# Optimization experiments

Measured on AMD Instinct MI355X. Metric: run time of the kernel, lower is better.

## Reference

```python
import jax, jax.numpy as jnp
import numpy as np

HEADS = 8
DIM_HEAD = 64
CHUNK = 128
EPS = 1e-6
KERNEL_EPS = 1e-4


def softmax_kernel(x, proj, is_query):
    # x: [b,h,n,d], proj: [f,d]  (FAVOR+ positive softmax features)
    d = x.shape[-1]
    data_normalizer = d ** -0.25
    ratio = proj.shape[0] ** -0.5
    data_dash = jnp.einsum('bhnd,fd->bhnf', x * data_normalizer, proj)
    diag = 0.5 * (data_normalizer ** 2) * jnp.sum(x * x, axis=-1, keepdims=True)  # [b,h,n,1]
    if is_query:
        m = jnp.max(data_dash, axis=-1, keepdims=True)
    else:
        m = jnp.max(data_dash, axis=(-1, -2), keepdims=True)
    return ratio * (jnp.exp(data_dash - diag - jax.lax.stop_gradient(m)) + KERNEL_EPS)


def infer_hidden_states(q, k, v, chunk_size=CHUNK):
    # q,k: [b,h,n,f], v: [b,h,n,e]; chunked causal linear attention with carried cumsums
    b, h, n, f = q.shape
    e = v.shape[-1]
    nc = n // chunk_size

    def to_chunks(t):
        return jnp.moveaxis(t.reshape(b, h, nc, chunk_size, t.shape[-1]), 2, 0)

    qs, ks, vs = to_chunks(q), to_chunks(k), to_chunks(v)

    def step(carry, inp):
        Z, S = carry  # [b,h,1,f], [b,h,1,f,e]
        qc, kc, vc = inp
        k_cum = Z + jnp.cumsum(kc, axis=2)                       # [b,h,c,f]
        D_inv = 1.0 / jnp.einsum('bhnf,bhnf->bhn', qc, k_cum + EPS)
        ctx = jnp.einsum('bhnf,bhne->bhnfe', kc, vc)             # [b,h,c,f,e]
        ctx_cum = S + jnp.cumsum(ctx, axis=2)
        out = jnp.einsum('bhnfe,bhnf,bhn->bhne', ctx_cum, qc, D_inv)
        return (k_cum[:, :, -1:], ctx_cum[:, :, -1:]), out

    init = (jnp.zeros((b, h, 1, f), q.dtype), jnp.zeros((b, h, 1, f, e), q.dtype))
    (Z, S), outs = jax.lax.scan(step, init, (qs, ks, vs))
    out = jnp.moveaxis(outs, 0, 2).reshape(b, h, n, e)
    return out, Z[:, :, 0], S[:, :, 0]


def reference(x, proj, Wq, Wk, Wv, Wo, bo):
    b, n, dim = x.shape
    h, dh = HEADS, DIM_HEAD

    def split_heads(t):
        return jnp.transpose(t.reshape(b, n, h, dh), (0, 2, 1, 3))

    q = split_heads(x @ Wq)
    k = split_heads(x @ Wk)
    v = split_heads(x @ Wv)

    qf = softmax_kernel(q, proj, is_query=True)
    kf = softmax_kernel(k, proj, is_query=False)

    out, Z, S = infer_hidden_states(qf, kf, v)
    out = jnp.transpose(out, (0, 2, 1, 3)).reshape(b, n, h * dh)
    out = out @ Wo + bo
    return out, Z, S


def setup_inputs() -> dict:
    key = jax.random.key(0)
    ks = jax.random.split(key, 6)
    b, n, dim = 2, 2048, 512
    f = 256
    return {
        'x': jax.random.normal(ks[0], (b, n, dim), jnp.float32),
        'proj': jax.random.normal(ks[1], (f, DIM_HEAD), jnp.float32),
        'Wq': jax.random.normal(ks[2], (dim, dim), jnp.float32) * (dim ** -0.5),
        'Wk': jax.random.normal(ks[3], (dim, dim), jnp.float32) * (dim ** -0.5),
        'Wv': jax.random.normal(ks[4], (dim, dim), jnp.float32) * (dim ** -0.5),
        'Wo': jax.random.normal(ks[5], (dim, dim), jnp.float32) * (dim ** -0.5),
        'bo': jnp.zeros((dim,), jnp.float32),
    }
```

## Files before the change

### kernel.cpp

```cpp
#include <hip/hip_runtime.h>
#include <hip/hip_bf16.h>
#include <math.h>

#define NB    2
#define NSEQ  2048
#define DIMM  512
#define NH    8
#define DHd   64
#define FF    256
#define CHK   128
#define NCHK  16
#define NBH   16

typedef unsigned short ushort_t;
typedef __attribute__((ext_vector_type(8))) __bf16 bf16x8;
typedef __attribute__((ext_vector_type(4))) float floatx4;

__device__ __forceinline__ unsigned short f2bf(float x) {
    union { __hip_bfloat16 h; unsigned short u; } v;
    v.h = __float2bfloat16(x);
    return v.u;
}
__device__ __forceinline__ float bf2f(unsigned short u) {
    union { unsigned short u2[2]; float f; } v;
    v.u2[0] = 0; v.u2[1] = u;
    return v.f;
}
__device__ __forceinline__ unsigned enc_f(float x) {
    unsigned u = __float_as_uint(x);
    return (u & 0x80000000u) ? ~u : (u | 0x80000000u);
}
__device__ __forceinline__ float dec_f(unsigned e) {
    unsigned u = (e & 0x80000000u) ? (e & 0x7fffffffu) : ~e;
    return __uint_as_float(u);
}

__device__ __forceinline__ void gload16(const void* g, void* l) {
    __builtin_amdgcn_global_load_lds(
        (const __attribute__((address_space(1))) void*)g,
        (__attribute__((address_space(3))) void*)l, 16, 0, 0);
}

__device__ __forceinline__ bf16x8 frag8(const ushort_t* lds, int row, int kb) {
    return *((const bf16x8*)lds + row * 8 + (kb ^ (row & 7)));
}
__device__ __forceinline__ bf16x8 fragS(const ushort_t* lds, int row, int kb) {
    return *((const bf16x8*)lds + row * 16 + (kb ^ (row & 15)));
}

__global__ __launch_bounds__(256)
void prep(const float* __restrict__ x, const float* __restrict__ proj,
          const float* __restrict__ W0, const float* __restrict__ W1,
          const float* __restrict__ W2, const float* __restrict__ W3,
          ushort_t* __restrict__ xb, ushort_t* __restrict__ projb,
          ushort_t* __restrict__ T0, ushort_t* __restrict__ T1,
          ushort_t* __restrict__ T2, ushort_t* __restrict__ T3,
          unsigned* __restrict__ mk_u)
{
    __shared__ float t[32][33];
    const int b = blockIdx.x, tid = threadIdx.x;
    if (b < 2048) {
        const int gid = b * 256 + tid;
        const float4 v = *(const float4*)(x + (size_t)gid * 4);
        union { ushort4 v4; unsigned short s[4]; } pk;
        pk.s[0] = f2bf(v.x); pk.s[1] = f2bf(v.y); pk.s[2] = f2bf(v.z); pk.s[3] = f2bf(v.w);
        ((ushort4*)xb)[gid] = pk.v4;
    } else if (b < 2064) {
        const int gid = (b - 2048) * 256 + tid;
        const float dn = 0.35355339059327379f;
        const float4 v = *(const float4*)(proj + (size_t)gid * 4);
        union { ushort4 v4; unsigned short s[4]; } pk;
        pk.s[0] = f2bf(v.x * dn); pk.s[1] = f2bf(v.y * dn);
        pk.s[2] = f2bf(v.z * dn); pk.s[3] = f2bf(v.w * dn);
        ((ushort4*)projb)[gid] = pk.v4;
    } else if (b < 3088) {
        const int idx = b - 2064;
        const int z = idx >> 8, rem = idx & 255;
        const int bx = rem & 15, by = rem >> 4;
        const float* W = (z == 0) ? W0 : (z == 1) ? W1 : (z == 2) ? W2 : W3;
        ushort_t* T = (z == 0) ? T0 : (z == 1) ? T1 : (z == 2) ? T2 : T3;
        const int x0 = bx * 32, y0 = by * 32;
        const int tx = tid & 31, ty = tid >> 5;
#pragma unroll
        for (int i = 0; i < 4; i++)
            t[ty + i * 8][tx] = W[(size_t)(y0 + ty + i * 8) * DIMM + x0 + tx];
        __syncthreads();
#pragma unroll
        for (int i = 0; i < 4; i++)
            T[(size_t)(x0 + ty + i * 8) * DIMM + y0 + tx] = f2bf(t[tx][ty + i * 8]);
    } else {
        if (tid < NBH) mk_u[tid] = 0u;
    }
}

__device__ __forceinline__ void mfma_mainloop(
    const ushort_t* __restrict__ AG, const ushort_t* __restrict__ BG,
    ushort_t* As, ushort_t* Bs, int ldA, int ldB, int K,
    floatx4 acc[4][4], int tid)
{
    const int lane = tid & 63, wid = tid >> 6;
    const int q = lane >> 4, c = lane & 15;
    const int wm = (wid >> 1) * 64, wn = (wid & 1) * 64;

    for (int k0 = 0; k0 < K; k0 += 64) {
#pragma unroll
        for (int t = 0; t < 4; t++) {
            const int g = t * 256 + tid, r = g >> 3, kb = (g & 7) ^ (r & 7);
            gload16(AG + (size_t)r * ldA + k0 + kb * 8, As + (size_t)g * 8);
        }
#pragma unroll
        for (int t = 0; t < 4; t++) {
            const int g = t * 256 + tid, r = g >> 3, kb = (g & 7) ^ (r & 7);
            gload16(BG + (size_t)r * ldB + k0 + kb * 8, Bs + (size_t)g * 8);
        }
        __syncthreads();
#pragma unroll
        for (int ks = 0; ks < 2; ks++) {
            bf16x8 af[4], bfr[4];
#pragma unroll
            for (int i = 0; i < 4; i++) {
                af[i]  = frag8(As, wm + i * 16 + c, ks * 4 + q);
                bfr[i] = frag8(Bs, wn + i * 16 + c, ks * 4 + q);
            }
#pragma unroll
            for (int i = 0; i < 4; i++)
#pragma unroll
                for (int j = 0; j < 4; j++)
                    acc[i][j] = __builtin_amdgcn_mfma_f32_16x16x32_bf16(
                        af[i], bfr[j], acc[i][j], 0, 0, 0);
        }
        __syncthreads();
    }
}

__global__ __launch_bounds__(256)
void gemm_qkv(const ushort_t* __restrict__ xb,
              const ushort_t* __restrict__ Wtq, const ushort_t* __restrict__ Wtk,
              const ushort_t* __restrict__ Wtv,
              ushort_t* __restrict__ qb, ushort_t* __restrict__ kb,
              ushort_t* __restrict__ vTb)
{
    __shared__ alignas(16) ushort_t SM[16640];
    ushort_t* As = SM;
    ushort_t* Bs = SM + 8192;
    const int tid = threadIdx.x;
    const int n0 = blockIdx.x * 128, m0 = blockIdx.y * 128, z = blockIdx.z;
    const ushort_t* Bt = (z == 0) ? Wtq : ((z == 1) ? Wtk : Wtv);

    floatx4 zero = {0.f, 0.f, 0.f, 0.f};
    floatx4 acc[4][4];
#pragma unroll
    for (int i = 0; i < 4; i++)
#pragma unroll
        for (int j = 0; j < 4; j++) acc[i][j] = zero;

    mfma_mainloop(xb + (size_t)m0 * DIMM, Bt + (size_t)n0 * DIMM, As, Bs,
                  DIMM, DIMM, DIMM, acc, tid);

    const int lane = tid & 63, wid = tid >> 6;
    const int q = lane >> 4, c = lane & 15;
    const int wm = (wid >> 1) * 64, wn = (wid & 1) * 64;
    if (z < 2) {
        ushort_t* ob = (z == 0) ? qb : kb;
#pragma unroll
        for (int i = 0; i < 4; i++)
#pragma unroll
            for (int j = 0; j < 4; j++) {
                const int col = n0 + wn + j * 16 + c;
#pragma unroll
                for (int r = 0; r < 4; r++) {
                    const int row = m0 + wm + i * 16 + q * 4 + r;
                    ob[(size_t)row * DIMM + col] = f2bf(acc[i][j][r]);
                }
            }
    } else {
#pragma unroll
        for (int i = 0; i < 4; i++)
#pragma unroll
            for (int j = 0; j < 4; j++) {
                const int col = wn + j * 16 + c;
#pragma unroll
                for (int r = 0; r < 4; r++) {
                    const int row = wm + i * 16 + q * 4 + r;
                    SM[row * 130 + col] = f2bf(acc[i][j][r]);
                }
            }
        __syncthreads();
        const int bb = m0 >> 11, nbase = m0 & 2047;
#pragma unroll
        for (int p = 0; p < 16; p++) {
            const int idx = p * 256 + tid;
            const int cl2 = idx >> 5, n4 = idx & 31;
            const int C = n0 + cl2;
            const int h = C >> 6, e = C & 63;
            union { ushort4 v4; unsigned short s[4]; } pk;
#pragma unroll
            for (int k = 0; k < 4; k++) pk.s[k] = SM[(n4 * 4 + k) * 130 + cl2];
            *(ushort4*)(vTb + (((size_t)(bb * NH + h) * 64 + e)) * NSEQ + nbase + n4 * 4) = pk.v4;
        }
    }
}

__global__ __launch_bounds__(256)
void gemm_out(const ushort_t* __restrict__ attnb, const ushort_t* __restrict__ Wto,
              float* __restrict__ out, const float* __restrict__ bias)
{
    __shared__ alignas(16) ushort_t As[8192];
    __shared__ alignas(16) ushort_t Bs[8192];
    const int tid = threadIdx.x;
    const int n0 = blockIdx.x * 128, m0 = blockIdx.y * 128;

    floatx4 zero = {0.f, 0.f, 0.f, 0.f};
    floatx4 acc[4][4];
#pragma unroll
    for (int i = 0; i < 4; i++)
#pragma unroll
        for (int j = 0; j < 4; j++) acc[i][j] = zero;

    mfma_mainloop(attnb + (size_t)m0 * DIMM, Wto + (size_t)n0 * DIMM, As, Bs,
                  DIMM, DIMM, DIMM, acc, tid);

    const int lane = tid & 63, wid = tid >> 6;
    const int q = lane >> 4, c = lane & 15;
    const int wm = (wid >> 1) * 64, wn = (wid & 1) * 64;
#pragma unroll
    for (int i = 0; i < 4; i++)
#pragma unroll
        for (int j = 0; j < 4; j++) {
            const int col = n0 + wn + j * 16 + c;
            const float bv = bias[col];
#pragma unroll
            for (int r = 0; r < 4; r++) {
                const int row = m0 + wm + i * 16 + q * 4 + r;
                out[(size_t)row * DIMM + col] = acc[i][j][r] + bv;
            }
        }
}

__global__ __launch_bounds__(256)
void feat_qk(const ushort_t* __restrict__ qb_, const ushort_t* __restrict__ kb_,
             const ushort_t* __restrict__ projb,
             ushort_t* __restrict__ qfb, float* __restrict__ ddk,
             unsigned* __restrict__ mk_u)
{
    __shared__ alignas(16) ushort_t As[8192];
    __shared__ alignas(16) ushort_t Bs[16384];
    __shared__ float dtmp[256];
    __shared__ float diag_l[128];
    __shared__ float mx2[2][128];
    __shared__ float red[256];
    const int tid = threadIdx.x, lane = tid & 63, wid = tid >> 6;
    const int q = lane >> 4, cl = lane & 15;
    const int m0 = blockIdx.x * 128, h = blockIdx.y, src = blockIdx.z;
    const int bb = m0 >> 11, nloc = m0 & 2047;
    const ushort_t* Aq = (src ? kb_ : qb_) + (size_t)m0 * DIMM + h * 64;

    if (src == 0) {
        const int row = tid >> 1, half = tid & 1;
        float s = 0.f;
        const ushort_t* p = Aq + (size_t)row * DIMM + half * 32;
#pragma unroll
        for (int d = 0; d < 32; d += 4) {
            ushort4 w = *(const ushort4*)(p + d);
            float a = bf2f(w.x), b2 = bf2f(w.y), c2 = bf2f(w.z), d2 = bf2f(w.w);
            s += a * a + b2 * b2 + c2 * c2 + d2 * d2;
        }
        dtmp[tid] = s;
        __syncthreads();
        if (tid < 128) diag_l[tid] = (dtmp[tid * 2] + dtmp[tid * 2 + 1]) * 0.0625f;
    }

    floatx4 zero = {0.f, 0.f, 0.f, 0.f};
    floatx4 acc[4][8];
#pragma unroll
    for (int i = 0; i < 4; i++)
#pragma unroll
        for (int j = 0; j < 8; j++) acc[i][j] = zero;

    const int wm = (wid >> 1) * 64, wn = (wid & 1) * 128;
#pragma unroll
    for (int t = 0; t < 4; t++) {
        const int g = t * 256 + tid, r = g >> 3, kb = (g & 7) ^ (r & 7);
        gload16(Aq + (size_t)r * DIMM + kb * 8, As + (size_t)g * 8);
    }
#pragma unroll
    for (int t = 0; t < 8; t++) {
        const int g = t * 256 + tid, r = g >> 3, kb = (g & 7) ^ (r & 7);
        gload16(projb + (size_t)r * 64 + kb * 8, Bs + (size_t)g * 8);
    }
    __syncthreads();
#pragma unroll
    for (int ks = 0; ks < 2; ks++) {
        bf16x8 af[4], bfr[8];
#pragma unroll
        for (int i = 0; i < 4; i++) af[i] = frag8(As, wm + i * 16 + cl, ks * 4 + q);
#pragma unroll
        for (int j = 0; j < 8; j++) bfr[j] = frag8(Bs, wn + j * 16 + cl, ks * 4 + q);
#pragma unroll
        for (int i = 0; i < 4; i++)
#pragma unroll
            for (int j = 0; j < 8; j++)
                acc[i][j] = __builtin_amdgcn_mfma_f32_16x16x32_bf16(
                    af[i], bfr[j], acc[i][j], 0, 0, 0);
    }

    if (src == 0) {
#pragma unroll
        for (int i = 0; i < 4; i++)
#pragma unroll
            for (int r = 0; r < 4; r++) {
                const int row = wm + i * 16 + q * 4 + r;
                float mx = -3.0e38f;
#pragma unroll
                for (int j = 0; j < 8; j++) mx = fmaxf(mx, acc[i][j][r]);
                mx = fmaxf(mx, __shfl_xor(mx, 1)); mx = fmaxf(mx, __shfl_xor(mx, 2));
                mx = fmaxf(mx, __shfl_xor(mx, 4)); mx = fmaxf(mx, __shfl_xor(mx, 8));
                if (cl == 0) mx2[wid & 1][row] = mx;
            }
        __syncthreads();
#pragma unroll
        for (int i = 0; i < 4; i++)
#pragma unroll
            for (int r = 0; r < 4; r++) {
                const int row = wm + i * 16 + q * 4 + r;
                const float cc = diag_l[row] + fmaxf(mx2[0][row], mx2[1][row]);
#pragma unroll
                for (int j = 0; j < 8; j++) {
                    const int col = wn + j * 16 + cl;
                    const float v = 0.0625f * (__expf(acc[i][j][r] - cc) + 1.0e-4f);
                    qfb[((size_t)(bb * NH + h) * NSEQ + (nloc + row)) * FF + col] = f2bf(v);
                }
            }
    } else {
        float mloc = -3.0e38f;
#pragma unroll
        for (int i = 0; i < 4; i++)
#pragma unroll
            for (int j = 0; j < 8; j++) {
                const int f = wn + j * 16 + cl;
#pragma unroll
                for (int r = 0; r < 4; r++) {
                    const int row = wm + i * 16 + q * 4 + r;
                    const float v = acc[i][j][r];
                    mloc = fmaxf(mloc, v);
                    ddk[((size_t)(bb * NH + h) * NSEQ + (nloc + row)) * FF + f] = v;
                }
            }
        red[tid] = mloc;
        __syncthreads();
        for (int s = 128; s > 0; s >>= 1) {
            if (tid < s) red[tid] = fmaxf(red[tid], red[tid + s]);
            __syncthreads();
        }
        if (tid == 0) atomicMax(&mk_u[bb * NH + h], enc_f(red[0]));
    }
}

__global__ __launch_bounds__(256)
void exp_tk(const float* __restrict__ ddk, const ushort_t* __restrict__ kb_,
            const unsigned* __restrict__ mk_u,
            ushort_t* __restrict__ kfb, ushort_t* __restrict__ kfTb,
            float* __restrict__ Ksum)
{
    __shared__ ushort_t t[64][136];
    __shared__ float red[4][64];
    __shared__ float dtmp[256];
    __shared__ float diag_l[128];
    const int tid = threadIdx.x;
    const int f0 = blockIdx.x * 64, c = blockIdx.y, bh = blockIdx.z;
    const int bb = bh >> 3, h = bh & 7;
    const int n0 = c * CHK;
    const float m = dec_f(mk_u[bh]);

    {
        const int row = tid >> 1, half = tid & 1;
        float s = 0.f;
        const ushort_t* p = kb_ + (size_t)(bb * NSEQ + n0 + row) * DIMM + h * 64 + half * 32;
#pragma unroll
        for (int d = 0; d < 32; d += 4) {
            ushort4 w = *(const ushort4*)(p + d);
            float a = bf2f(w.x), b2 = bf2f(w.y), c2 = bf2f(w.z), d2 = bf2f(w.w);
            s += a * a + b2 * b2 + c2 * c2 + d2 * d2;
        }
        dtmp[tid] = s;
    }
    __syncthreads();
    if (tid < 128) diag_l[tid] = (dtmp[tid * 2] + dtmp[tid * 2 + 1]) * 0.0625f;
    __syncthreads();

#pragma unroll
    for (int p = 0; p < 8; p++) {
        const int idx = p * 256 + tid;
        const int row = idx >> 4, c4 = idx & 15;
        const float4 d4 = *(const float4*)(ddk + ((size_t)(bh * NSEQ + n0 + row)) * FF + f0 + c4 * 4);
        const float cc = diag_l[row] + m;
        union { ushort4 v4; unsigned short s[4]; } pk;
        pk.s[0] = f2bf(0.0625f * (__expf(d4.x - cc) + 1.0e-4f));
        pk.s[1] = f2bf(0.0625f * (__expf(d4.y - cc) + 1.0e-4f));
        pk.s[2] = f2bf(0.0625f * (__expf(d4.z - cc) + 1.0e-4f));
        pk.s[3] = f2bf(0.0625f * (__expf(d4.w - cc) + 1.0e-4f));
        *(ushort4*)(kfb + ((size_t)(bh * NSEQ + n0 + row)) * FF + f0 + c4 * 4) = pk.v4;
        t[c4 * 4 + 0][row] = pk.s[0]; t[c4 * 4 + 1][row] = pk.s[1];
        t[c4 * 4 + 2][row] = pk.s[2]; t[c4 * 4 + 3][row] = pk.s[3];
    }
    __syncthreads();
    {
        const int f = tid & 63, grp = tid >> 6;
        float s = 0.f;
#pragma unroll
        for (int n = 0; n < 32; n++) s += bf2f(t[f][grp * 32 + n]);
        red[grp][f] = s;
    }
    __syncthreads();
    if (tid < 64)
        Ksum[((size_t)bh * NCHK + c) * FF + f0 + tid] =
            red[0][tid] + red[1][tid] + red[2][tid] + red[3][tid];
#pragma unroll
    for (int p = 0; p < 8; p++) {
        const int idx = p * 256 + tid;
        const int f = idx >> 5, n4 = idx & 31;
        ushort4 o = *(const ushort4*)&t[f][n4 * 4];
        *(ushort4*)(kfTb + ((size_t)(bh * FF + f0 + f)) * NSEQ + n0 + n4 * 4) = o;
    }
}

__global__ __launch_bounds__(256)
void ctx_mfma(const ushort_t* __restrict__ vTb, const ushort_t* __restrict__ kfTb,
              float* __restrict__ CTXT)
{
    __shared__ alignas(16) ushort_t As[4096];
    __shared__ alignas(16) ushort_t Bs[16384];
    const int tid = threadIdx.x, lane = tid & 63, wid = tid >> 6;
    const int q = lane >> 4, cl = lane & 15;
    const int bh = blockIdx.x >> 4, c = blockIdx.x & 15;
    const ushort_t* A = vTb + ((size_t)bh * 64) * NSEQ + c * CHK;
    const ushort_t* B = kfTb + ((size_t)bh * FF) * NSEQ + c * CHK;
    const int fw = wid * 64;

    floatx4 zero = {0.f, 0.f, 0.f, 0.f};
    floatx4 acc[4][4];
#pragma unroll
    for (int i = 0; i < 4; i++)
#pragma unroll
        for (int j = 0; j < 4; j++) acc[i][j] = zero;

    for (int k0 = 0; k0 < CHK; k0 += 64) {
#pragma unroll
        for (int t = 0; t < 2; t++) {
            const int g = t * 256 + tid, r = g >> 3, kb = (g & 7) ^ (r & 7);
            gload16(A + (size_t)r * NSEQ + k0 + kb * 8, As + (size_t)g * 8);
        }
#pragma unroll
        for (int t = 0; t < 8; t++) {
            const int g = t * 256 + tid, r = g >> 3, kb = (g & 7) ^ (r & 7);
            gload16(B + (size_t)r * NSEQ + k0 + kb * 8, Bs + (size_t)g * 8);
        }
        __syncthreads();
#pragma unroll
        for (int ks = 0; ks < 2; ks++) {
            bf16x8 af[4], bfr[4];
#pragma unroll
            for (int i = 0; i < 4; i++) {
                af[i]  = frag8(As, i * 16 + cl, ks * 4 + q);
                bfr[i] = frag8(Bs, fw + i * 16 + cl, ks * 4 + q);
            }
#pragma unroll
            for (int i = 0; i < 4; i++)
#pragma unroll
                for (int j = 0; j < 4; j++)
                    acc[i][j] = __builtin_amdgcn_mfma_f32_16x16x32_bf16(
                        af[i], bfr[j], acc[i][j], 0, 0, 0);
        }
        __syncthreads();
    }
#pragma unroll
    for (int i = 0; i < 4; i++)
#pragma unroll
        for (int j = 0; j < 4; j++) {
            const int f = fw + j * 16 + cl;
#pragma unroll
            for (int r = 0; r < 4; r++) {
                const int e = i * 16 + q * 4 + r;
                CTXT[(((size_t)bh * NCHK + c) * 64 + e) * FF + f] = acc[i][j][r];
            }
        }
}

__global__ void prefix_zs(float* __restrict__ Ksum, float* __restrict__ Zout,
                          const float* __restrict__ CTXT, ushort_t* __restrict__ ctxp,
                          float* __restrict__ Sout)
{
    const int b = blockIdx.x;
    if (b < 1024) {
        const int idx = b * 256 + threadIdx.x;
        const int bh = idx >> 14, ef = idx & 16383;
        const int e = ef >> 8, f = ef & 255;
        float run = 0.f;
#pragma unroll
        for (int c = 0; c < NCHK; c++) {
            const size_t o = (((size_t)bh * NCHK + c) * 64 + e) * FF + f;
            const float t = CTXT[o];
            ctxp[o] = f2bf(run);
            run += t;
        }
        Sout[((size_t)bh * FF + f) * 64 + e] = run;
    } else {
        const int idx = (b - 1024) * 256 + threadIdx.x;
        const int bh = idx >> 8, f = idx & 255;
        float run = 0.f;
#pragma unroll
        for (int c = 0; c < NCHK; c++) {
            const size_t o = ((size_t)(bh * NCHK + c)) * FF + f;
            const float t = Ksum[o];
            Ksum[o] = run;
            run += t;
        }
        Zout[(size_t)bh * FF + f] = run;
    }
}

__global__ __launch_bounds__(256)
void chunk_out_mfma(const ushort_t* __restrict__ qfb, const ushort_t* __restrict__ kfb,
                    const ushort_t* __restrict__ vTb, const float* __restrict__ Zex,
                    const ushort_t* __restrict__ ctxp, ushort_t* __restrict__ attnb)
{
    __shared__ alignas(16) ushort_t Sld[16384];
    __shared__ alignas(16) ushort_t As[8192];
    __shared__ alignas(16) ushort_t Bs[8192];
    __shared__ float zeps[256];
    __shared__ float rows_part[2][128];
    __shared__ float denp[256];
    __shared__ float den_l[128];

    const int tid = threadIdx.x, lane = tid & 63, wid = tid >> 6;
    const int q = lane >> 4, cl = lane & 15;
    const int bh = blockIdx.x >> 4, c = blockIdx.x & 15;
    const int bb = bh >> 3, h = bh & 7;
    const int n0 = c * CHK;
    const ushort_t* Q  = qfb + ((size_t)bh * NSEQ + n0) * FF;
    const ushort_t* Kf = kfb + ((size_t)bh * NSEQ + n0) * FF;

    zeps[tid] = Zex[((size_t)bh * NCHK + c) * FF + tid] + 1.0e-6f;

    floatx4 zero = {0.f, 0.f, 0.f, 0.f};
    floatx4 acc1[4][4];
#pragma unroll
    for (int i = 0; i < 4; i++)
#pragma unroll
        for (int j = 0; j < 4; j++) acc1[i][j] = zero;
    const int wm = (wid >> 1) * 64, wn = (wid & 1) * 64;
    for (int k0 = 0; k0 < FF; k0 += 64) {
#pragma unroll
        for (int t = 0; t < 4; t++) {
            const int g = t * 256 + tid, r = g >> 3, kb = (g & 7) ^ (r & 7);
            gload16(Q + (size_t)r * FF + k0 + kb * 8, As + (size_t)g * 8);
        }
#pragma unroll
        for (int t = 0; t < 4; t++) {
            const int g = t * 256 + tid, r = g >> 3, kb = (g & 7) ^ (r & 7);
            gload16(Kf + (size_t)r * FF + k0 + kb * 8, Bs + (size_t)g * 8);
        }
        __syncthreads();
#pragma unroll
        for (int ks = 0; ks < 2; ks++) {
            bf16x8 af[4], bfr[4];
#pragma unroll
            for (int i = 0; i < 4; i++) {
                af[i]  = frag8(As, wm + i * 16 + cl, ks * 4 + q);
                bfr[i] = frag8(Bs, wn + i * 16 + cl, ks * 4 + q);
            }
#pragma unroll
            for (int i = 0; i < 4; i++)
#pragma unroll
                for (int j = 0; j < 4; j++)
                    acc1[i][j] = __builtin_amdgcn_mfma_f32_16x16x32_bf16(
                        af[i], bfr[j], acc1[i][j], 0, 0, 0);
        }
        __syncthreads();
    }
#pragma unroll
    for (int i = 0; i < 4; i++)
#pragma unroll
        for (int r = 0; r < 4; r++) {
            const int row = wm + i * 16 + q * 4 + r;
            float part = 0.f;
#pragma unroll
            for (int j = 0; j < 4; j++) {
                const int col = wn + j * 16 + cl;
                const float v = (col <= row) ? acc1[i][j][r] : 0.f;
                part += v;
                Sld[(row * 16 + ((col >> 3) ^ (row & 15))) * 8 + (col & 7)] = f2bf(v);
            }
            part += __shfl_xor(part, 1); part += __shfl_xor(part, 2);
            part += __shfl_xor(part, 4); part += __shfl_xor(part, 8);
            if (cl == 0) rows_part[wid & 1][row] = part;
        }
    __syncthreads();

    floatx4 acc2[4][2];
#pragma unroll
    for (int i = 0; i < 4; i++)
#pragma unroll
        for (int j = 0; j < 2; j++) acc2[i][j] = zero;
    const ushort_t* Vt = vTb + ((size_t)bh * 64) * NSEQ + n0;
    for (int k0 = 0; k0 < CHK; k0 += 64) {
#pragma unroll
        for (int t = 0; t < 2; t++) {
            const int g = t * 256 + tid, r = g >> 3, kb = (g & 7) ^ (r & 7);
            gload16(Vt + (size_t)r * NSEQ + k0 + kb * 8, As + (size_t)g * 8);
        }
        __syncthreads();
#pragma unroll
        for (int ks = 0; ks < 2; ks++) {
            bf16x8 af[4], bfr[2];
            const int kbS = (k0 >> 3) + ks * 4 + q;
#pragma unroll
            for (int i = 0; i < 4; i++) af[i] = frag8(As, i * 16 + cl, ks * 4 + q);
#pragma unroll
            for (int j = 0; j < 2; j++) bfr[j] = fragS(Sld, wid * 32 + j * 16 + cl, kbS);
#pragma unroll
            for (int i = 0; i < 4; i++)
#pragma unroll
                for (int j = 0; j < 2; j++)
                    acc2[i][j] = __builtin_amdgcn_mfma_f32_16x16x32_bf16(
                        af[i], bfr[j], acc2[i][j], 0, 0, 0);
        }
        __syncthreads();
    }

    const ushort_t* Cp = ctxp + ((size_t)bh * NCHK + c) * 64 * FF;
    float dacc = 0.f;
    const int drow = tid & 127, dhalf = tid >> 7;
    for (int k0 = 0; k0 < FF; k0 += 64) {
#pragma unroll
        for (int t = 0; t < 2; t++) {
            const int g = t * 256 + tid, r = g >> 3, kb = (g & 7) ^ (r & 7);
            gload16(Cp + (size_t)r * FF + k0 + kb * 8, As + (size_t)g * 8);
        }
#pragma unroll
        for (int t = 0; t < 4; t++) {
            const int g = t * 256 + tid, r = g >> 3, kb = (g & 7) ^ (r & 7);
            gload16(Q + (size_t)r * FF + k0 + kb * 8, Bs + (size_t)g * 8);
        }
        __syncthreads();
#pragma unroll
        for (int ks = 0; ks < 2; ks++) {
            bf16x8 af[4], bfr[2];
#pragma unroll
            for (int i = 0; i < 4; i++) af[i] = frag8(As, i * 16 + cl, ks * 4 + q);
#pragma unroll
            for (int j = 0; j < 2; j++) bfr[j] = frag8(Bs, wid * 32 + j * 16 + cl, ks * 4 + q);
#pragma unroll
            for (int i = 0; i < 4; i++)
#pragma unroll
                for (int j = 0; j < 2; j++)
                    acc2[i][j] = __builtin_amdgcn_mfma_f32_16x16x32_bf16(
                        af[i], bfr[j], acc2[i][j], 0, 0, 0);
        }
#pragma unroll
        for (int gi = 0; gi < 4; gi++) {
            const int kb = dhalf * 4 + gi;
            const ushort_t* gp = Bs + ((size_t)drow * 8 + (kb ^ (drow & 7))) * 8;
            const int kbase = k0 + kb * 8;
#pragma unroll
            for (int e2 = 0; e2 < 8; e2++)
                dacc = fmaf(bf2f(gp[e2]), zeps[kbase + e2], dacc);
        }
        __syncthreads();
    }
    denp[tid] = dacc;
    __syncthreads();
    if (tid < 128)
        den_l[tid] = rows_part[0][tid] + rows_part[1][tid] + denp[tid] + denp[tid + 128];
    __syncthreads();

#pragma unroll
    for (int j = 0; j < 2; j++) {
        const int row = wid * 32 + j * 16 + cl;
        const float dinv = 1.0f / den_l[row];
#pragma unroll
        for (int i = 0; i < 4; i++)
#pragma unroll
            for (int r = 0; r < 4; r++) {
                const int e = i * 16 + q * 4 + r;
                Sld[row * 68 + e] = f2bf(acc2[i][j][r] * dinv);
            }
    }
    __syncthreads();
#pragma unroll
    for (int p = 0; p < 8; p++) {
        const int idx = p * 256 + tid;
        const int row = idx >> 4, e4 = idx & 15;
        ushort4 o = *(const ushort4*)&Sld[row * 68 + e4 * 4];
        *(ushort4*)(attnb + ((size_t)(bb * NSEQ + n0 + row)) * DIMM + h * 64 + e4 * 4) = o;
    }
}

extern "C" void kernel_launch(void* const* d_in, const int* in_sizes, int n_in,
                              void* d_out, int out_size, void* d_ws, size_t ws_size,
                              hipStream_t stream)
{
    (void)in_sizes; (void)n_in; (void)out_size; (void)ws_size;
    const float* x    = (const float*)d_in[0];
    const float* proj = (const float*)d_in[1];
    const float* Wq   = (const float*)d_in[2];
    const float* Wk   = (const float*)d_in[3];
    const float* Wv   = (const float*)d_in[4];
    const float* Wo   = (const float*)d_in[5];
    const float* bo   = (const float*)d_in[6];
    float* out = (float*)d_out;

    char* W = (char*)d_ws;
    float*    ddk  = (float*)W;              W += (size_t)33554432;
    ushort_t* kfTb = (ushort_t*)W;           W += (size_t)16777216;
    ushort_t* qfb  = (ushort_t*)W;           W += (size_t)16777216;
    ushort_t* kfb  = (ushort_t*)W;           W += (size_t)16777216;
    ushort_t* qb   = (ushort_t*)W;           W += (size_t)4194304;
    ushort_t* kb   = (ushort_t*)W;           W += (size_t)4194304;
    ushort_t* xb   = (ushort_t*)W;           W += (size_t)4194304;
    ushort_t* vTb  = (ushort_t*)W;           W += (size_t)4194304;
    ushort_t* Wtq  = (ushort_t*)W;           W += (size_t)524288;
    ushort_t* Wtk  = (ushort_t*)W;           W += (size_t)524288;
    ushort_t* Wtv  = (ushort_t*)W;           W += (size_t)524288;
    ushort_t* Wto  = (ushort_t*)W;           W += (size_t)524288;
    ushort_t* projb = (ushort_t*)W;          W += (size_t)32768;
    float*    Ksum = (float*)W;              W += (size_t)262144;
    unsigned* mk_u = (unsigned*)W;           W += (size_t)256;

    float*    CTXT = ddk;
    ushort_t* ctxp = qb;
    ushort_t* attnb = xb;

    float* Zout = out + (size_t)4096 * 512;
    float* Sout = Zout + (size_t)NBH * FF;

    hipLaunchKernelGGL(prep, dim3(3089), dim3(256), 0, stream,
                       x, proj, Wq, Wk, Wv, Wo, xb, projb, Wtq, Wtk, Wtv, Wto, mk_u);
    hipLaunchKernelGGL(gemm_qkv, dim3(4, 32, 3), dim3(256), 0, stream,
                       xb, Wtq, Wtk, Wtv, qb, kb, vTb);
    hipLaunchKernelGGL(feat_qk, dim3(32, 8, 2), dim3(256), 0, stream,
                       qb, kb, projb, qfb, ddk, mk_u);
    hipLaunchKernelGGL(exp_tk, dim3(4, 16, 16), dim3(256), 0, stream,
                       ddk, kb, mk_u, kfb, kfTb, Ksum);
    hipLaunchKernelGGL(ctx_mfma, dim3(256), dim3(256), 0, stream, vTb, kfTb, CTXT);
    hipLaunchKernelGGL(prefix_zs, dim3(1040), dim3(256), 0, stream,
                       Ksum, Zout, CTXT, ctxp, Sout);
    hipLaunchKernelGGL(chunk_out_mfma, dim3(256), dim3(256), 0, stream,
                       qfb, kfb, vTb, Ksum, ctxp, attnb);
    hipLaunchKernelGGL(gemm_out, dim3(4, 32), dim3(256), 0, stream, attnb, Wto, out, bo);
}
```

Measured before the change: 168.6 us.

## Recompute key projections instead of storing fp32 logits; stage GEMM epilogue through LDS

Feature stage restructured. A new kmax kernel computes the key projection only to find the global per-head max. A fused featx kernel then recomputes the projection for both q and k, applies the exp, and writes qf, kf, the transposed kf and per-chunk Ksum through an LDS-staged coalesced epilogue. This removes the 32 MB fp32 ddk round-trip and the separate exp_tk kernel, at the cost of a second small MFMA pass over K. The QKV GEMM epilogue also now stages q/k through shared memory for vectorized coalesced stores.

After: 165.7 us. About the same (-1.7%).

```diff
diff --git a/kernel.cpp b/kernel.cpp
--- a/kernel.cpp
+++ b/kernel.cpp
@@ -140,7 +140,7 @@
               ushort_t* __restrict__ qb, ushort_t* __restrict__ kb,
               ushort_t* __restrict__ vTb)
 {
-    __shared__ alignas(16) ushort_t SM[16640];
+    __shared__ alignas(16) ushort_t SM[16896];
     ushort_t* As = SM;
     ushort_t* Bs = SM + 8192;
     const int tid = threadIdx.x;
@@ -160,32 +160,30 @@
     const int lane = tid & 63, wid = tid >> 6;
     const int q = lane >> 4, c = lane & 15;
     const int wm = (wid >> 1) * 64, wn = (wid & 1) * 64;
+
+#pragma unroll
+    for (int i = 0; i < 4; i++)
+#pragma unroll
+        for (int j = 0; j < 4; j++) {
+            const int col = wn + j * 16 + c;
+#pragma unroll
+            for (int r = 0; r < 4; r++) {
+                const int row = wm + i * 16 + q * 4 + r;
+                SM[row * 132 + col] = f2bf(acc[i][j][r]);
+            }
+        }
+    __syncthreads();
+
     if (z < 2) {
         ushort_t* ob = (z == 0) ? qb : kb;
 #pragma unroll
-        for (int i = 0; i < 4; i++)
-#pragma unroll
-            for (int j = 0; j < 4; j++) {
-                const int col = n0 + wn + j * 16 + c;
-#pragma unroll
-                for (int r = 0; r < 4; r++) {
-                    const int row = m0 + wm + i * 16 + q * 4 + r;
-                    ob[(size_t)row * DIMM + col] = f2bf(acc[i][j][r]);
-                }
-            }
+        for (int p = 0; p < 16; p++) {
+            const int idx = p * 256 + tid;
+            const int row = idx >> 5, c4 = idx & 31;
+            ushort4 o = *(const ushort4*)&SM[row * 132 + c4 * 4];
+            *(ushort4*)(ob + (size_t)(m0 + row) * DIMM + n0 + c4 * 4) = o;
+        }
     } else {
-#pragma unroll
-        for (int i = 0; i < 4; i++)
-#pragma unroll
-            for (int j = 0; j < 4; j++) {
-                const int col = wn + j * 16 + c;
-#pragma unroll
-                for (int r = 0; r < 4; r++) {
-                    const int row = wm + i * 16 + q * 4 + r;
-                    SM[row * 130 + col] = f2bf(acc[i][j][r]);
-                }
-            }
-        __syncthreads();
         const int bb = m0 >> 11, nbase = m0 & 2047;
 #pragma unroll
         for (int p = 0; p < 16; p++) {
@@ -195,7 +193,7 @@
             const int h = C >> 6, e = C & 63;
             union { ushort4 v4; unsigned short s[4]; } pk;
 #pragma unroll
-            for (int k = 0; k < 4; k++) pk.s[k] = SM[(n4 * 4 + k) * 130 + cl2];
+            for (int k = 0; k < 4; k++) pk.s[k] = SM[(n4 * 4 + k) * 132 + cl2];
             *(ushort4*)(vTb + (((size_t)(bb * NH + h) * 64 + e)) * NSEQ + nbase + n4 * 4) = pk.v4;
         }
     }
@@ -238,24 +236,89 @@
 }
 
 __global__ __launch_bounds__(256)
-void feat_qk(const ushort_t* __restrict__ qb_, const ushort_t* __restrict__ kb_,
-             const ushort_t* __restrict__ projb,
-             ushort_t* __restrict__ qfb, float* __restrict__ ddk,
-             unsigned* __restrict__ mk_u)
+void kmax(const ushort_t* __restrict__ kb_, const ushort_t* __restrict__ projb,
+          unsigned* __restrict__ mk_u)
 {
     __shared__ alignas(16) ushort_t As[8192];
     __shared__ alignas(16) ushort_t Bs[16384];
+    __shared__ float red[256];
+    const int tid = threadIdx.x, lane = tid & 63, wid = tid >> 6;
+    const int q = lane >> 4, cl = lane & 15;
+    const int m0 = blockIdx.x * 128, h = blockIdx.y;
+    const int bb = m0 >> 11;
+    const ushort_t* Aq = kb_ + (size_t)m0 * DIMM + h * 64;
+
+#pragma unroll
+    for (int t = 0; t < 4; t++) {
+        const int g = t * 256 + tid, r = g >> 3, kb = (g & 7) ^ (r & 7);
+        gload16(Aq + (size_t)r * DIMM + kb * 8, As + (size_t)g * 8);
+    }
+#pragma unroll
+    for (int t = 0; t < 8; t++) {
+        const int g = t * 256 + tid, r = g >> 3, kb = (g & 7) ^ (r & 7);
+        gload16(projb + (size_t)r * 64 + kb * 8, Bs + (size_t)g * 8);
+    }
+    __syncthreads();
+
+    floatx4 zero = {0.f, 0.f, 0.f, 0.f};
+    floatx4 acc[4][8];
+#pragma unroll
+    for (int i = 0; i < 4; i++)
+#pragma unroll
+        for (int j = 0; j < 8; j++) acc[i][j] = zero;
+    const int wm = (wid >> 1) * 64, wn = (wid & 1) * 128;
+#pragma unroll
+    for (int ks = 0; ks < 2; ks++) {
+        bf16x8 af[4], bfr[8];
+#pragma unroll
+        for (int i = 0; i < 4; i++) af[i] = frag8(As, wm + i * 16 + cl, ks * 4 + q);
+#pragma unroll
+        for (int j = 0; j < 8; j++) bfr[j] = frag8(Bs, wn + j * 16 + cl, ks * 4 + q);
+#pragma unroll
+        for (int i = 0; i < 4; i++)
+#pragma unroll
+            for (int j = 0; j < 8; j++)
+                acc[i][j] = __builtin_amdgcn_mfma_f32_16x16x32_bf16(
+                    af[i], bfr[j], acc[i][j], 0, 0, 0);
+    }
+    float mloc = -3.0e38f;
+#pragma unroll
+    for (int i = 0; i < 4; i++)
+#pragma unroll
+        for (int j = 0; j < 8; j++)
+#pragma unroll
+            for (int r = 0; r < 4; r++) mloc = fmaxf(mloc, acc[i][j][r]);
+    red[tid] = mloc;
+    __syncthreads();
+    for (int s = 128; s > 0; s >>= 1) {
+        if (tid < s) red[tid] = fmaxf(red[tid], red[tid + s]);
+        __syncthreads();
+    }
+    if (tid == 0) atomicMax(&mk_u[bb * NH + h], enc_f(red[0]));
+}
+
+__global__ __launch_bounds__(256)
+void featx(const ushort_t* __restrict__ qb_, const ushort_t* __restrict__ kb_,
+           const ushort_t* __restrict__ projb, const unsigned* __restrict__ mk_u,
+           ushort_t* __restrict__ qfb, ushort_t* __restrict__ kfb,
+           ushort_t* __restrict__ kfTb, float* __restrict__ Ksum)
+{
+    __shared__ alignas(16) ushort_t SM[24576];
     __shared__ float dtmp[256];
     __shared__ float diag_l[128];
     __shared__ float mx2[2][128];
-    __shared__ float red[256];
+    __shared__ float colp[2][256];
+    ushort_t* As = SM;
+    ushort_t* Bs = SM + 8192;
     const int tid = threadIdx.x, lane = tid & 63, wid = tid >> 6;
     const int q = lane >> 4, cl = lane & 15;
     const int m0 = blockIdx.x * 128, h = blockIdx.y, src = blockIdx.z;
     const int bb = m0 >> 11, nloc = m0 & 2047;
+    const int bh = bb * NH + h;
+    const int cidx = nloc >> 7;
     const ushort_t* Aq = (src ? kb_ : qb_) + (size_t)m0 * DIMM + h * 64;
 
-    if (src == 0) {
+    {
         const int row = tid >> 1, half = tid & 1;
         float s = 0.f;
         const ushort_t* p = Aq + (size_t)row * DIMM + half * 32;
@@ -266,18 +329,10 @@
             s += a * a + b2 * b2 + c2 * c2 + d2 * d2;
         }
         dtmp[tid] = s;
-        __syncthreads();
-        if (tid < 128) diag_l[tid] = (dtmp[tid * 2] + dtmp[tid * 2 + 1]) * 0.0625f;
-    }
-
-    floatx4 zero = {0.f, 0.f, 0.f, 0.f};
-    floatx4 acc[4][8];
-#pragma unroll
-    for (int i = 0; i < 4; i++)
-#pragma unroll
-        for (int j = 0; j < 8; j++) acc[i][j] = zero;
-
-    const int wm = (wid >> 1) * 64, wn = (wid & 1) * 128;
+    }
+    __syncthreads();
+    if (tid < 128) diag_l[tid] = (dtmp[2 * tid] + dtmp[2 * tid + 1]) * 0.0625f;
+
 #pragma unroll
     for (int t = 0; t < 4; t++) {
         const int g = t * 256 + tid, r = g >> 3, kb = (g & 7) ^ (r & 7);
@@ -289,6 +344,14 @@
         gload16(projb + (size_t)r * 64 + kb * 8, Bs + (size_t)g * 8);
     }
     __syncthreads();
+
+    floatx4 zero = {0.f, 0.f, 0.f, 0.f};
+    floatx4 acc[4][8];
+#pragma unroll
+    for (int i = 0; i < 4; i++)
+#pragma unroll
+        for (int j = 0; j < 8; j++) acc[i][j] = zero;
+    const int wm = (wid >> 1) * 64, wn = (wid & 1) * 128;
 #pragma unroll
     for (int ks = 0; ks < 2; ks++) {
         bf16x8 af[4], bfr[8];
@@ -304,6 +367,7 @@
                     af[i], bfr[j], acc[i][j], 0, 0, 0);
     }
 
+    const float mk = src ? dec_f(mk_u[bh]) : 0.f;
     if (src == 0) {
 #pragma unroll
         for (int i = 0; i < 4; i++)
@@ -317,110 +381,74 @@
                 mx = fmaxf(mx, __shfl_xor(mx, 4)); mx = fmaxf(mx, __shfl_xor(mx, 8));
                 if (cl == 0) mx2[wid & 1][row] = mx;
             }
-        __syncthreads();
-#pragma unroll
-        for (int i = 0; i < 4; i++)
-#pragma unroll
-            for (int r = 0; r < 4; r++) {
-                const int row = wm + i * 16 + q * 4 + r;
-                const float cc = diag_l[row] + fmaxf(mx2[0][row], mx2[1][row]);
+    }
+    __syncthreads();
+
+#pragma unroll
+    for (int i = 0; i < 4; i++)
+#pragma unroll
+        for (int r = 0; r < 4; r++) {
+            const int row = wm + i * 16 + q * 4 + r;
+            const float cc = diag_l[row] + (src ? mk : fmaxf(mx2[0][row], mx2[1][row]));
+#pragma unroll
+            for (int j = 0; j < 8; j++)
+                acc[i][j][r] = 0.0625f * (__expf(acc[i][j][r] - cc) + 1.0e-4f);
+        }
+
+    if (src) {
+#pragma unroll
+        for (int j = 0; j < 8; j++) {
+            float s = 0.f;
+#pragma unroll
+            for (int i = 0; i < 4; i++)
+                s += acc[i][j][0] + acc[i][j][1] + acc[i][j][2] + acc[i][j][3];
+            s += __shfl_xor(s, 16);
+            s += __shfl_xor(s, 32);
+            if (q == 0) colp[wid >> 1][wn + j * 16 + cl] = s;
+        }
+    }
+
+    ushort_t* ff = src ? kfb : qfb;
+    const size_t frow = (size_t)bh * NSEQ + nloc;
+
+#pragma unroll
+    for (int hf = 0; hf < 2; hf++) {
+        __syncthreads();
+        if ((wid & 1) == hf) {
+#pragma unroll
+            for (int i = 0; i < 4; i++)
 #pragma unroll
                 for (int j = 0; j < 8; j++) {
-                    const int col = wn + j * 16 + cl;
-                    const float v = 0.0625f * (__expf(acc[i][j][r] - cc) + 1.0e-4f);
-                    qfb[((size_t)(bb * NH + h) * NSEQ + (nloc + row)) * FF + col] = f2bf(v);
+                    const int col = j * 16 + cl;
+#pragma unroll
+                    for (int r = 0; r < 4; r++) {
+                        const int row = wm + i * 16 + q * 4 + r;
+                        SM[row * 132 + col] = f2bf(acc[i][j][r]);
+                    }
                 }
-            }
-    } else {
-        float mloc = -3.0e38f;
-#pragma unroll
-        for (int i = 0; i < 4; i++)
-#pragma unroll
-            for (int j = 0; j < 8; j++) {
-                const int f = wn + j * 16 + cl;
-#pragma unroll
-                for (int r = 0; r < 4; r++) {
-                    const int row = wm + i * 16 + q * 4 + r;
-                    const float v = acc[i][j][r];
-                    mloc = fmaxf(mloc, v);
-                    ddk[((size_t)(bb * NH + h) * NSEQ + (nloc + row)) * FF + f] = v;
-                }
-            }
-        red[tid] = mloc;
-        __syncthreads();
-        for (int s = 128; s > 0; s >>= 1) {
-            if (tid < s) red[tid] = fmaxf(red[tid], red[tid + s]);
-            __syncthreads();
-        }
-        if (tid == 0) atomicMax(&mk_u[bb * NH + h], enc_f(red[0]));
-    }
-}
-
-__global__ __launch_bounds__(256)
-void exp_tk(const float* __restrict__ ddk, const ushort_t* __restrict__ kb_,
-            const unsigned* __restrict__ mk_u,
-            ushort_t* __restrict__ kfb, ushort_t* __restrict__ kfTb,
-            float* __restrict__ Ksum)
-{
-    __shared__ ushort_t t[64][136];
-    __shared__ float red[4][64];
-    __shared__ float dtmp[256];
-    __shared__ float diag_l[128];
-    const int tid = threadIdx.x;
-    const int f0 = blockIdx.x * 64, c = blockIdx.y, bh = blockIdx.z;
-    const int bb = bh >> 3, h = bh & 7;
-    const int n0 = c * CHK;
-    const float m = dec_f(mk_u[bh]);
-
-    {
-        const int row = tid >> 1, half = tid & 1;
-        float s = 0.f;
-        const ushort_t* p = kb_ + (size_t)(bb * NSEQ + n0 + row) * DIMM + h * 64 + half * 32;
-#pragma unroll
-        for (int d = 0; d < 32; d += 4) {
-            ushort4 w = *(const ushort4*)(p + d);
-            float a = bf2f(w.x), b2 = bf2f(w.y), c2 = bf2f(w.z), d2 = bf2f(w.w);
-            s += a * a + b2 * b2 + c2 * c2 + d2 * d2;
-        }
-        dtmp[tid] = s;
-    }
-    __syncthreads();
-    if (tid < 128) diag_l[tid] = (dtmp[tid * 2] + dtmp[tid * 2 + 1]) * 0.0625f;
-    __syncthreads();
-
-#pragma unroll
-    for (int p = 0; p < 8; p++) {
-        const int idx = p * 256 + tid;
-        const int row = idx >> 4, c4 = idx & 15;
-        const float4 d4 = *(const float4*)(ddk + ((size_t)(bh * NSEQ + n0 + row)) * FF + f0 + c4 * 4);
-        const float cc = diag_l[row] + m;
-        union { ushort4 v4; unsigned short s[4]; } pk;
-        pk.s[0] = f2bf(0.0625f * (__expf(d4.x - cc) + 1.0e-4f));
-        pk.s[1] = f2bf(0.0625f * (__expf(d4.y - cc) + 1.0e-4f));
-        pk.s[2] = f2bf(0.0625f * (__expf(d4.z - cc) + 1.0e-4f));
-        pk.s[3] = f2bf(0.0625f * (__expf(d4.w - cc) + 1.0e-4f));
-        *(ushort4*)(kfb + ((size_t)(bh * NSEQ + n0 + row)) * FF + f0 + c4 * 4) = pk.v4;
-        t[c4 * 4 + 0][row] = pk.s[0]; t[c4 * 4 + 1][row] = pk.s[1];
-        t[c4 * 4 + 2][row] = pk.s[2]; t[c4 * 4 + 3][row] = pk.s[3];
-    }
-    __syncthreads();
-    {
-        const int f = tid & 63, grp = tid >> 6;
-        float s = 0.f;
-#pragma unroll
-        for (int n = 0; n < 32; n++) s += bf2f(t[f][grp * 32 + n]);
-        red[grp][f] = s;
-    }
-    __syncthreads();
-    if (tid < 64)
-        Ksum[((size_t)bh * NCHK + c) * FF + f0 + tid] =
-            red[0][tid] + red[1][tid] + red[2][tid] + red[3][tid];
-#pragma unroll
-    for (int p = 0; p < 8; p++) {
-        const int idx = p * 256 + tid;
-        const int f = idx >> 5, n4 = idx & 31;
-        ushort4 o = *(const ushort4*)&t[f][n4 * 4];
-        *(ushort4*)(kfTb + ((size_t)(bh * FF + f0 + f)) * NSEQ + n0 + n4 * 4) = o;
+        }
+        if (hf == 0 && src) {
+            Ksum[((size_t)bh * NCHK + cidx) * FF + tid] = colp[0][tid] + colp[1][tid];
+        }
+        __syncthreads();
+#pragma unroll
+        for (int p = 0; p < 16; p++) {
+            const int idx = p * 256 + tid;
+            const int row = idx >> 5, c4 = idx & 31;
+            ushort4 o = *(const ushort4*)&SM[row * 132 + c4 * 4];
+            *(ushort4*)(ff + (frow + row) * FF + hf * 128 + c4 * 4) = o;
+        }
+        if (src) {
+#pragma unroll
+            for (int p = 0; p < 16; p++) {
+                const int idx = p * 256 + tid;
+                const int f = idx >> 5, n4 = idx & 31;
+                union { ushort4 v4; unsigned short s[4]; } pk;
+#pragma unroll
+                for (int k = 0; k < 4; k++) pk.s[k] = SM[(n4 * 4 + k) * 132 + f];
+                *(ushort4*)(kfTb + ((size_t)bh * FF + hf * 128 + f) * NSEQ + nloc + n4 * 4) = pk.v4;
+            }
+        }
     }
 }
 
@@ -711,7 +739,7 @@
     float* out = (float*)d_out;
 
     char* W = (char*)d_ws;
-    float*    ddk  = (float*)W;              W += (size_t)33554432;
+    float*    CTXT = (float*)W;              W += (size_t)16777216;
     ushort_t* kfTb = (ushort_t*)W;           W += (size_t)16777216;
     ushort_t* qfb  = (ushort_t*)W;           W += (size_t)16777216;
     ushort_t* kfb  = (ushort_t*)W;           W += (size_t)16777216;
@@ -727,7 +755,6 @@
     float*    Ksum = (float*)W;              W += (size_t)262144;
     unsigned* mk_u = (unsigned*)W;           W += (size_t)256;
 
-    float*    CTXT = ddk;
     ushort_t* ctxp = qb;
     ushort_t* attnb = xb;
 
@@ -738,10 +765,9 @@
                        x, proj, Wq, Wk, Wv, Wo, xb, projb, Wtq, Wtk, Wtv, Wto, mk_u);
     hipLaunchKernelGGL(gemm_qkv, dim3(4, 32, 3), dim3(256), 0, stream,
                        xb, Wtq, Wtk, Wtv, qb, kb, vTb);
-    hipLaunchKernelGGL(feat_qk, dim3(32, 8, 2), dim3(256), 0, stream,
-                       qb, kb, projb, qfb, ddk, mk_u);
-    hipLaunchKernelGGL(exp_tk, dim3(4, 16, 16), dim3(256), 0, stream,
-                       ddk, kb, mk_u, kfb, kfTb, Ksum);
+    hipLaunchKernelGGL(kmax, dim3(32, 8), dim3(256), 0, stream, kb, projb, mk_u);
+    hipLaunchKernelGGL(featx, dim3(32, 8, 2), dim3(256), 0, stream,
+                       qb, kb, projb, mk_u, qfb, kfb, kfTb, Ksum);
     hipLaunchKernelGGL(ctx_mfma, dim3(256), dim3(256), 0, stream, vTb, kfTb, CTXT);
     hipLaunchKernelGGL(prefix_zs, dim3(1040), dim3(256), 0, stream,
                        Ksum, Zout, CTXT, ctxp, Sout);
```
